# Kernel optimization log

Hardware: AMD Instinct MI355X
Metric: run time of the kernel (lower is better)

Reference implementation:

```python
import jax, jax.numpy as jnp
import numpy as np

DIM = 2048
BATCH = 16384
EPS = 1e-12


def setup_inputs() -> dict:
    key = jax.random.key(0)
    ks = jax.random.split(key, 12)
    d = DIM
    inp = {
        "h_final": jax.random.normal(ks[0], (BATCH, d), dtype=jnp.float32),
        "v_claim": jax.random.normal(ks[1], (BATCH, d), dtype=jnp.float32),
        "v_doc": jax.random.normal(ks[2], (BATCH, d), dtype=jnp.float32),
        # feature_extractor: Linear(d+3, d) -> ReLU -> Linear(d, d//2) -> ReLU
        "W1": jax.random.normal(ks[3], (d + 3, d), dtype=jnp.float32) / np.sqrt(d + 3),
        "b1": jnp.zeros((d,), dtype=jnp.float32),
        "W2": jax.random.normal(ks[4], (d, d // 2), dtype=jnp.float32) / np.sqrt(d),
        "b2": jnp.zeros((d // 2,), dtype=jnp.float32),
        # retrieval head: Linear(d//2, 1) -> Sigmoid
        "Wr": jax.random.normal(ks[5], (d // 2, 1), dtype=jnp.float32) / np.sqrt(d // 2),
        "br": jnp.zeros((1,), dtype=jnp.float32),
    }
    return inp


def reference(h_final, v_claim, v_doc, W1, b1, W2, b2, Wr, br):
    # L2-normalize claim/doc vectors (F.normalize with eps clamp)
    cn = v_claim / jnp.maximum(jnp.linalg.norm(v_claim, axis=-1, keepdims=True), EPS)
    dn = v_doc / jnp.maximum(jnp.linalg.norm(v_doc, axis=-1, keepdims=True), EPS)
    # alignment = cosine similarity (vectors already unit norm) -> [B, 1]
    align = jnp.sum(cn * dn, axis=-1, keepdims=True)
    # divergence = 1 - alignment; tension = divergence^2
    div = 1.0 - align
    tens = div * div
    features = jnp.concatenate([h_final, align, div, tens], axis=-1)  # [B, d+3]
    h = jax.nn.relu(features @ W1 + b1)
    shared = jax.nn.relu(h @ W2 + b2)  # [B, d//2]
    out = jax.nn.sigmoid(shared @ Wr + br)  # [B, 1] (task='retrieval')
    return out
```

## Files before the change

kernel.cpp:

```cpp
#include <hip/hip_runtime.h>
#include <hip/hip_bf16.h>
#include <stdint.h>

#define BATCH 16384
#define DIM   2048
#define DIM2  1024

typedef __attribute__((ext_vector_type(8))) short short8;
typedef __attribute__((ext_vector_type(4))) float f32x4;

__device__ __forceinline__ ushort f2bf(float f) {
  uint32_t u = __float_as_uint(f);
  u += 0x7fffu + ((u >> 16) & 1u);
  return (ushort)(u >> 16);
}
__device__ __forceinline__ float bf2f(ushort h) {
  return __uint_as_float(((uint32_t)h) << 16);
}

__device__ __forceinline__ void gload_lds16(const void* g, void* l) {
  __builtin_amdgcn_global_load_lds(
      (__attribute__((address_space(1))) void*)g,
      (__attribute__((address_space(3))) void*)l,
      16, 0, 0);
}

__device__ __forceinline__ f32x4 MFMA(short8 a, short8 b, f32x4 c) {
  return __builtin_amdgcn_mfma_f32_16x16x32_bf16(a, b, c, 0, 0, 0);
}

__global__ void __launch_bounds__(256) prep_fused(const float* __restrict__ vc,
                                                  const float* __restrict__ vd,
                                                  const float* __restrict__ h,
                                                  ushort* __restrict__ hbf,
                                                  float* __restrict__ feats) {
  const int w = threadIdx.x >> 6, l = threadIdx.x & 63;
  const int row = blockIdx.x * 4 + w;
  const float4* c  = (const float4*)(vc + (size_t)row * DIM);
  const float4* d  = (const float4*)(vd + (size_t)row * DIM);
  const float4* hp = (const float4*)(h  + (size_t)row * DIM);
  float dot = 0.f, c2 = 0.f, d2 = 0.f;
  float4 hv[8];
#pragma unroll
  for (int j = 0; j < 8; ++j) {
    float4 a = c[j * 64 + l];
    float4 b = d[j * 64 + l];
    hv[j] = hp[j * 64 + l];
    dot += a.x * b.x + a.y * b.y + a.z * b.z + a.w * b.w;
    c2  += a.x * a.x + a.y * a.y + a.z * a.z + a.w * a.w;
    d2  += b.x * b.x + b.y * b.y + b.z * b.z + b.w * b.w;
  }
  uint2* ho = (uint2*)(hbf + (size_t)row * DIM);
#pragma unroll
  for (int j = 0; j < 8; ++j) {
    uint2 u;
    u.x = (uint32_t)f2bf(hv[j].x) | ((uint32_t)f2bf(hv[j].y) << 16);
    u.y = (uint32_t)f2bf(hv[j].z) | ((uint32_t)f2bf(hv[j].w) << 16);
    ho[j * 64 + l] = u;
  }
#pragma unroll
  for (int off = 32; off >= 1; off >>= 1) {
    dot += __shfl_xor(dot, off, 64);
    c2  += __shfl_xor(c2, off, 64);
    d2  += __shfl_xor(d2, off, 64);
  }
  if (l == 0) {
    float nc = fmaxf(sqrtf(c2), 1e-12f);
    float nd = fmaxf(sqrtf(d2), 1e-12f);
    float align = dot / (nc * nd);
    float dv = 1.f - align;
    feats[row] = align;
    feats[BATCH + row] = dv;
    feats[2 * BATCH + row] = dv * dv;
  }
}

__global__ void __launch_bounds__(256) transW(const float* __restrict__ W,
                                              ushort* __restrict__ WT,
                                              int K, int N) {
  __shared__ float tile[32][33];
  int t = threadIdx.x;
  int tx = t & 31, ty = t >> 5;
  int c0 = blockIdx.x * 32, r0 = blockIdx.y * 32;
#pragma unroll
  for (int p = 0; p < 4; ++p)
    tile[ty + p * 8][tx] = W[(size_t)(r0 + ty + p * 8) * N + c0 + tx];
  __syncthreads();
#pragma unroll
  for (int p = 0; p < 4; ++p) {
    int rr = ty + p * 8;
    WT[(size_t)(c0 + rr) * K + r0 + tx] = f2bf(tile[tx][rr]);
  }
}

template <int MODE, int N>
__global__ void __launch_bounds__(512, 1) gemm256(const ushort* __restrict__ A,
                                                  const ushort* __restrict__ BT,
                                                  ushort* __restrict__ C,
                                                  const float* __restrict__ feats,
                                                  const float* __restrict__ wex,
                                                  const float* __restrict__ bias) {
  constexpr int K = 2048;
  constexpr int NT = K / 64;
  __shared__ __align__(16) char lds[131072];
  const int tid = threadIdx.x;
  const int l = tid & 63, w = tid >> 6;
  const int wr = w >> 2, wc = w & 3;
  const int l4 = l & 15, lhi = l >> 4;

  constexpr int GX = N / 256;
  const int bid = blockIdx.x;
  const int xcd = bid & 7;
  const int s = bid >> 3;
  const int tx = s % GX;
  const int ty = xcd * 8 + s / GX;
  const size_t rowBase = (size_t)ty * 256;
  const int colBase = tx * 256;

  const int swz = (l4 & 7) << 4;
  const int aoffBase = l4 * 128 + ((wr * 64 + lhi * 16) ^ swz);
  const int boffBase = ((wc & 1) * 64 + l4) * 128 + (((wc >> 1) * 64 + lhi * 16) ^ swz);

  const char* pAs[2];
  const char* pBs[2];
#pragma unroll
  for (int c = 0; c < 2; ++c) {
    int o = c * 8192 + tid * 16;
    int r = o >> 7, b0 = o & 127;
    int bsw = b0 ^ ((r & 7) << 4);
    int hb = bsw >> 6, cb = bsw & 63;
    pAs[c] = (const char*)A + (rowBase + hb * 128 + r) * (2 * K) + cb;
    pBs[c] = (const char*)BT + ((size_t)colBase + hb * 128 + r) * (2 * K) + cb;
  }
  const int ldso0 = w * 1024;
  const int ldso1 = 8192 + w * 1024;

#define STAGE(srcT, destPar, M, kh)                                          \
  do {                                                                       \
    char* dst_ = lds + (destPar) * 65536 + (kh) * 32768 + (M) * 16384;       \
    const char* s0_ = ((M) ? pBs[0] : pAs[0]) + (srcT) * 128 + (kh) * 64;    \
    const char* s1_ = ((M) ? pBs[1] : pAs[1]) + (srcT) * 128 + (kh) * 64;    \
    gload_lds16(s0_, dst_ + ldso0);                                          \
    gload_lds16(s1_, dst_ + ldso1);                                          \
    asm volatile("" ::: "memory");                                           \
  } while (0)

#define LOADA(q, d, kh)                                                      \
  do {                                                                       \
    const char* sb_ = lds + (d) * 65536 + (kh) * 32768;                      \
    aq[0] = *(const short8*)(sb_ + ((q) * 4 + 0) * 2048 + aoffBase);         \
    aq[1] = *(const short8*)(sb_ + ((q) * 4 + 1) * 2048 + aoffBase);         \
    aq[2] = *(const short8*)(sb_ + ((q) * 4 + 2) * 2048 + aoffBase);         \
    aq[3] = *(const short8*)(sb_ + ((q) * 4 + 3) * 2048 + aoffBase);         \
  } while (0)

#define LOADB(d, kh)                                                         \
  do {                                                                       \
    const char* sb_ = lds + (d) * 65536 + (kh) * 32768 + 16384;              \
    bq[0] = *(const short8*)(sb_ + 0 * 2048 + boffBase);                     \
    bq[1] = *(const short8*)(sb_ + 1 * 2048 + boffBase);                     \
    bq[2] = *(const short8*)(sb_ + 2 * 2048 + boffBase);                     \
    bq[3] = *(const short8*)(sb_ + 3 * 2048 + boffBase);                     \
  } while (0)

#define MF(q)                                                                \
  do {                                                                       \
    _Pragma("unroll") for (int j_ = 0; j_ < 4; ++j_)                         \
        _Pragma("unroll") for (int n_ = 0; n_ < 4; ++n_)                     \
            acc[(q) * 4 + j_][n_] = MFMA(aq[j_], bq[n_], acc[(q) * 4 + j_][n_]); \
  } while (0)

#define BAR()     __builtin_amdgcn_s_barrier()
#define MEMF()    asm volatile("" ::: "memory")
#define VM8()     asm volatile("s_waitcnt vmcnt(8)" ::: "memory")
#define PRIO(x)   __builtin_amdgcn_s_setprio(x)

  f32x4 acc[8][4];
#pragma unroll
  for (int i = 0; i < 8; ++i)
#pragma unroll
    for (int j = 0; j < 4; ++j) acc[i][j] = (f32x4){0.f, 0.f, 0.f, 0.f};

  STAGE(0, 0, 0, 0);
  STAGE(0, 0, 1, 0);
  STAGE(0, 0, 0, 1);
  STAGE(0, 0, 1, 1);
  STAGE(1, 1, 0, 0);
  STAGE(1, 1, 1, 0);
  VM8();
  BAR();
  MEMF();

  for (int I = 0; I < NT / 2; ++I) {
    const int o = 2 * I + 1;
    const int e2 = (2 * I + 2 < NT) ? 2 * I + 2 : 0;
    const int o2 = (2 * I + 3 < NT) ? 2 * I + 3 : 0;
    short8 aq[4], bq[4];
    LOADB(0, 0);
    LOADA(0, 0, 0);
    STAGE(o, 1, 0, 1);
    BAR(); MEMF();
    PRIO(1); MF(0); PRIO(0);
    BAR(); MEMF();
    LOADA(1, 0, 0);
    STAGE(o, 1, 1, 1);
    BAR(); MEMF();
    PRIO(1); MF(1); PRIO(0);
    VM8();
    BAR(); MEMF();
    LOADB(0, 1);
    LOADA(0, 0, 1);
    STAGE(e2, 0, 0, 0);
    BAR(); MEMF();
    PRIO(1); MF(0); PRIO(0);
    BAR(); MEMF();
    LOADA(1, 0, 1);
    STAGE(e2, 0, 1, 0);
    BAR(); MEMF();
    PRIO(1); MF(1); PRIO(0);
    VM8();
    BAR(); MEMF();
    LOADB(1, 0);
    LOADA(0, 1, 0);
    STAGE(e2, 0, 0, 1);
    BAR(); MEMF();
    PRIO(1); MF(0); PRIO(0);
    BAR(); MEMF();
    LOADA(1, 1, 0);
    STAGE(e2, 0, 1, 1);
    BAR(); MEMF();
    PRIO(1); MF(1); PRIO(0);
    VM8();
    BAR(); MEMF();
    LOADB(1, 1);
    LOADA(0, 1, 1);
    STAGE(o2, 1, 0, 0);
    BAR(); MEMF();
    PRIO(1); MF(0); PRIO(0);
    BAR(); MEMF();
    LOADA(1, 1, 1);
    STAGE(o2, 1, 1, 0);
    BAR(); MEMF();
    PRIO(1); MF(1); PRIO(0);
    VM8();
    BAR(); MEMF();
  }
  asm volatile("s_waitcnt vmcnt(0)" ::: "memory");

  int ccv[4];
  float bb[4], wa[4], wb2[4], wc3[4];
#pragma unroll
  for (int n = 0; n < 4; ++n) {
    int cc = colBase + wc * 64 + n * 16 + l4;
    ccv[n] = cc;
    bb[n] = bias[cc];
    if (MODE == 1) {
      wa[n] = wex[cc]; wb2[n] = wex[2048 + cc]; wc3[n] = wex[4096 + cc];
    } else {
      wa[n] = 0.f; wb2[n] = 0.f; wc3[n] = 0.f;
    }
  }
  const int lhi4 = lhi * 4;
#pragma unroll
  for (int m = 0; m < 8; ++m) {
#pragma unroll
    for (int r = 0; r < 4; ++r) {
      size_t rr = rowBase + wr * 128 + m * 16 + lhi4 + r;
      float f1 = 0.f, f2 = 0.f, f3 = 0.f;
      if (MODE == 1) {
        f1 = feats[rr]; f2 = feats[BATCH + rr]; f3 = feats[2 * BATCH + rr];
      }
#pragma unroll
      for (int n = 0; n < 4; ++n) {
        float v = acc[m][n][r] + bb[n];
        if (MODE == 1) v += f1 * wa[n] + f2 * wb2[n] + f3 * wc3[n];
        v = fmaxf(v, 0.f);
        C[rr * N + ccv[n]] = f2bf(v);
      }
    }
  }
#undef STAGE
#undef LOADA
#undef LOADB
#undef MF
#undef BAR
#undef MEMF
#undef VM8
#undef PRIO
}

__global__ void __launch_bounds__(256) head_kernel(const ushort* __restrict__ S,
                                                   const float* __restrict__ Wr,
                                                   const float* __restrict__ br,
                                                   float* __restrict__ out) {
  int row = blockIdx.x * 4 + (threadIdx.x >> 6);
  int l = threadIdx.x & 63;
  const ushort* s = S + (size_t)row * DIM2 + l * 16;
  const float4* wp = (const float4*)(Wr + l * 16);
  uint4 u0 = *(const uint4*)s;
  uint4 u1 = *(const uint4*)(s + 8);
  float4 w0 = wp[0], w1 = wp[1], w2 = wp[2], w3 = wp[3];
  float sum = 0.f;
  sum += bf2f((ushort)(u0.x & 0xffff)) * w0.x + bf2f((ushort)(u0.x >> 16)) * w0.y;
  sum += bf2f((ushort)(u0.y & 0xffff)) * w0.z + bf2f((ushort)(u0.y >> 16)) * w0.w;
  sum += bf2f((ushort)(u0.z & 0xffff)) * w1.x + bf2f((ushort)(u0.z >> 16)) * w1.y;
  sum += bf2f((ushort)(u0.w & 0xffff)) * w1.z + bf2f((ushort)(u0.w >> 16)) * w1.w;
  sum += bf2f((ushort)(u1.x & 0xffff)) * w2.x + bf2f((ushort)(u1.x >> 16)) * w2.y;
  sum += bf2f((ushort)(u1.y & 0xffff)) * w2.z + bf2f((ushort)(u1.y >> 16)) * w2.w;
  sum += bf2f((ushort)(u1.z & 0xffff)) * w3.x + bf2f((ushort)(u1.z >> 16)) * w3.y;
  sum += bf2f((ushort)(u1.w & 0xffff)) * w3.z + bf2f((ushort)(u1.w >> 16)) * w3.w;
#pragma unroll
  for (int off = 32; off >= 1; off >>= 1) sum += __shfl_down(sum, off, 64);
  if (l == 0) out[row] = 1.f / (1.f + expf(-(sum + br[0])));
}

extern "C" void kernel_launch(void* const* d_in, const int* in_sizes, int n_in,
                              void* d_out, int out_size, void* d_ws, size_t ws_size,
                              hipStream_t stream) {
  const float* h_final = (const float*)d_in[0];
  const float* v_claim = (const float*)d_in[1];
  const float* v_doc   = (const float*)d_in[2];
  const float* W1      = (const float*)d_in[3];
  const float* b1      = (const float*)d_in[4];
  const float* W2      = (const float*)d_in[5];
  const float* b2      = (const float*)d_in[6];
  const float* Wr      = (const float*)d_in[7];
  const float* br      = (const float*)d_in[8];
  float* out = (float*)d_out;

  char* ws = (char*)d_ws;
  ushort* Abf   = (ushort*)ws;
  ushort* Hbf   = (ushort*)(ws + 67108864);
  ushort* W1T   = (ushort*)(ws + 134217728);
  ushort* W2T   = (ushort*)(ws + 142606336);
  float*  feats = (float*)(ws + 146800640);
  ushort* Sbf   = Abf;

  prep_fused<<<BATCH / 4, 256, 0, stream>>>(v_claim, v_doc, h_final, Abf, feats);
  transW<<<dim3(DIM / 32, DIM / 32), 256, 0, stream>>>(W1, W1T, DIM, DIM);
  transW<<<dim3(DIM2 / 32, DIM / 32), 256, 0, stream>>>(W2, W2T, DIM, DIM2);

  gemm256<1, DIM><<<(DIM / 256) * (BATCH / 256), 512, 0, stream>>>(
      Abf, W1T, Hbf, feats, W1 + (size_t)2048 * 2048, b1);
  gemm256<2, DIM2><<<(DIM2 / 256) * (BATCH / 256), 512, 0, stream>>>(
      Hbf, W2T, Sbf, nullptr, nullptr, b2);

  head_kernel<<<BATCH / 4, 256, 0, stream>>>(Sbf, Wr, br, out);
}
```

Measured before the change: 288.0 us.

## Split prep into cosine and bf16-convert kernels; halve GEMM barriers

The fused prep kernel is split into a cosine-similarity kernel, which loads all claim and doc vectors up front, and a separate flat grid-strided fp32-to-bf16 conversion kernel for h_final. In the GEMM main loop, half of the workgroup barriers between LDS staging and MFMA phases are removed, leaving one barrier per phase. The split aims for better memory-level parallelism and fewer barrier stalls, at the cost of an extra kernel launch. Dropping barriers risks LDS read/write races if the remaining synchronisation does not fully order the staging writes against the fragment reads.

```diff
diff --git a/kernel.cpp b/kernel.cpp
--- a/kernel.cpp
+++ b/kernel.cpp
@@ -29,34 +29,25 @@
   return __builtin_amdgcn_mfma_f32_16x16x32_bf16(a, b, c, 0, 0, 0);
 }
 
-__global__ void __launch_bounds__(256) prep_fused(const float* __restrict__ vc,
+__global__ void __launch_bounds__(256) cos_kernel(const float* __restrict__ vc,
                                                   const float* __restrict__ vd,
-                                                  const float* __restrict__ h,
-                                                  ushort* __restrict__ hbf,
                                                   float* __restrict__ feats) {
   const int w = threadIdx.x >> 6, l = threadIdx.x & 63;
   const int row = blockIdx.x * 4 + w;
-  const float4* c  = (const float4*)(vc + (size_t)row * DIM);
-  const float4* d  = (const float4*)(vd + (size_t)row * DIM);
-  const float4* hp = (const float4*)(h  + (size_t)row * DIM);
+  const float4* c = (const float4*)(vc + (size_t)row * DIM);
+  const float4* d = (const float4*)(vd + (size_t)row * DIM);
+  float4 ca[8], da[8];
+#pragma unroll
+  for (int j = 0; j < 8; ++j) ca[j] = c[j * 64 + l];
+#pragma unroll
+  for (int j = 0; j < 8; ++j) da[j] = d[j * 64 + l];
   float dot = 0.f, c2 = 0.f, d2 = 0.f;
-  float4 hv[8];
 #pragma unroll
   for (int j = 0; j < 8; ++j) {
-    float4 a = c[j * 64 + l];
-    float4 b = d[j * 64 + l];
-    hv[j] = hp[j * 64 + l];
+    float4 a = ca[j], b = da[j];
     dot += a.x * b.x + a.y * b.y + a.z * b.z + a.w * b.w;
     c2  += a.x * a.x + a.y * a.y + a.z * a.z + a.w * a.w;
     d2  += b.x * b.x + b.y * b.y + b.z * b.z + b.w * b.w;
-  }
-  uint2* ho = (uint2*)(hbf + (size_t)row * DIM);
-#pragma unroll
-  for (int j = 0; j < 8; ++j) {
-    uint2 u;
-    u.x = (uint32_t)f2bf(hv[j].x) | ((uint32_t)f2bf(hv[j].y) << 16);
-    u.y = (uint32_t)f2bf(hv[j].z) | ((uint32_t)f2bf(hv[j].w) << 16);
-    ho[j * 64 + l] = u;
   }
 #pragma unroll
   for (int off = 32; off >= 1; off >>= 1) {
@@ -72,6 +63,24 @@
     feats[row] = align;
     feats[BATCH + row] = dv;
     feats[2 * BATCH + row] = dv * dv;
+  }
+}
+
+__global__ void __launch_bounds__(256) cvt_kernel(const float* __restrict__ in,
+                                                  ushort* __restrict__ out) {
+  const int i0 = blockIdx.x * 256 + threadIdx.x;
+  const int S = 8192 * 256;
+  const float4* p = (const float4*)in;
+  uint2* o = (uint2*)out;
+  float4 f[4];
+#pragma unroll
+  for (int j = 0; j < 4; ++j) f[j] = p[i0 + j * S];
+#pragma unroll
+  for (int j = 0; j < 4; ++j) {
+    uint2 u;
+    u.x = (uint32_t)f2bf(f[j].x) | ((uint32_t)f2bf(f[j].y) << 16);
+    u.y = (uint32_t)f2bf(f[j].z) | ((uint32_t)f2bf(f[j].w) << 16);
+    o[i0 + j * S] = u;
   }
 }
 
@@ -199,51 +208,43 @@
     LOADB(0, 0);
     LOADA(0, 0, 0);
     STAGE(o, 1, 0, 1);
-    BAR(); MEMF();
     PRIO(1); MF(0); PRIO(0);
-    BAR(); MEMF();
+    MEMF(); BAR(); MEMF();
     LOADA(1, 0, 0);
     STAGE(o, 1, 1, 1);
-    BAR(); MEMF();
     PRIO(1); MF(1); PRIO(0);
     VM8();
-    BAR(); MEMF();
+    MEMF(); BAR(); MEMF();
     LOADB(0, 1);
     LOADA(0, 0, 1);
     STAGE(e2, 0, 0, 0);
-    BAR(); MEMF();
     PRIO(1); MF(0); PRIO(0);
-    BAR(); MEMF();
+    MEMF(); BAR(); MEMF();
     LOADA(1, 0, 1);
     STAGE(e2, 0, 1, 0);
-    BAR(); MEMF();
     PRIO(1); MF(1); PRIO(0);
     VM8();
-    BAR(); MEMF();
+    MEMF(); BAR(); MEMF();
     LOADB(1, 0);
     LOADA(0, 1, 0);
     STAGE(e2, 0, 0, 1);
-    BAR(); MEMF();
     PRIO(1); MF(0); PRIO(0);
-    BAR(); MEMF();
+    MEMF(); BAR(); MEMF();
     LOADA(1, 1, 0);
     STAGE(e2, 0, 1, 1);
-    BAR(); MEMF();
     PRIO(1); MF(1); PRIO(0);
     VM8();
-    BAR(); MEMF();
+    MEMF(); BAR(); MEMF();
     LOADB(1, 1);
     LOADA(0, 1, 1);
     STAGE(o2, 1, 0, 0);
-    BAR(); MEMF();
     PRIO(1); MF(0); PRIO(0);
-    BAR(); MEMF();
+    MEMF(); BAR(); MEMF();
     LOADA(1, 1, 1);
     STAGE(o2, 1, 1, 0);
-    BAR(); MEMF();
     PRIO(1); MF(1); PRIO(0);
     VM8();
-    BAR(); MEMF();
+    MEMF(); BAR(); MEMF();
   }
   asm volatile("s_waitcnt vmcnt(0)" ::: "memory");
 
@@ -336,7 +337,8 @@
   float*  feats = (float*)(ws + 146800640);
   ushort* Sbf   = Abf;
 
-  prep_fused<<<BATCH / 4, 256, 0, stream>>>(v_claim, v_doc, h_final, Abf, feats);
+  cos_kernel<<<BATCH / 4, 256, 0, stream>>>(v_claim, v_doc, feats);
+  cvt_kernel<<<8192, 256, 0, stream>>>(h_final, Abf);
   transW<<<dim3(DIM / 32, DIM / 32), 256, 0, stream>>>(W1, W1T, DIM, DIM);
   transW<<<dim3(DIM2 / 32, DIM / 32), 256, 0, stream>>>(W2, W2T, DIM, DIM2);
 
```

Result: no change. 286.6 us (-0.5%).
